# Kernel optimization log

Measured on AMD Instinct MI355X. Metric: run time of the kernel, lower is better.

## Reference

```python
import jax, jax.numpy as jnp
import numpy as np

TAU = 1.0          # temperature
PAD = -1.0         # padded_value_indicator
MAX_ITER = 50      # sinkhorn iterations
NEG_BIG = -100000000.0


def setup_inputs() -> dict:
    key = jax.random.key(0)
    k1, k2 = jax.random.split(key)
    B, N = 128, 256
    y_pred = jax.random.normal(k1, (B, N), dtype=jnp.float32)
    y_true = jax.random.randint(k2, (B, N), 0, 5, dtype=jnp.int32)
    return {"y_pred": y_pred, "y_true": y_true}


def deterministic_neural_sort(s, tau, mask):
    # s: [B, n, 1], mask: [B, n] bool
    B, n = s.shape[0], s.shape[1]
    mor = mask[:, :, None] | mask[:, None, :]
    mand = mask[:, :, None] & mask[:, None, :]
    s = jnp.where(mask[:, :, None], NEG_BIG, s)
    A_s = jnp.abs(s - jnp.swapaxes(s, 1, 2))            # [B, n, n]
    A_s = jnp.where(mor, 0.0, A_s)
    # B_mat[b,i,j] = sum_k A_s[b,i,k] (matmul with ones outer product)
    B_mat = A_s.sum(axis=2, keepdims=True)              # [B, n, 1], broadcasts over j
    m = mask.sum(axis=1)                                # [B] number of padded items
    j = jnp.arange(n)
    valid = j[None, :] < (n - m)[:, None]
    scaling = jnp.where(
        valid,
        (n - m)[:, None].astype(jnp.float32) + 1.0 - 2.0 * (j[None, :] + 1).astype(jnp.float32),
        0.0,
    )                                                   # [B, n]
    s0 = jnp.where(mask[:, :, None], 0.0, s)
    C = s0 * scaling[:, None, :]                        # [B,n,1]*[B,1,n] outer product
    P_max = jnp.swapaxes(C - B_mat, 1, 2)
    P_max = jnp.where(mor, -jnp.inf, P_max)
    P_max = jnp.where(mand, 1.0, P_max)
    return jax.nn.softmax(P_max / tau, axis=-1)         # [B, n, n]


def sinkhorn_scaling(mat, mask):
    # mat: [B, n, n], mask: [B, n]
    mor = mask[:, None, :] | mask[:, :, None]
    mand = mask[:, None, :] & mask[:, :, None]
    mat = jnp.where(mor, 0.0, mat)
    mat = jnp.where(mand, 1.0, mat)

    def step(m, _):
        m = m / jnp.clip(m.sum(axis=1, keepdims=True), 1e-10, None)
        m = m / jnp.clip(m.sum(axis=2, keepdims=True), 1e-10, None)
        return m, None

    mat, _ = jax.lax.scan(step, mat, None, length=MAX_ITER)
    return jnp.where(mor, 0.0, mat)


def dcg_at_k(y_pred, y_true, k, gain_fn):
    # returns [B, 1]
    mask = y_true == PAD
    yp = jnp.where(mask, -jnp.inf, y_pred)
    yt = jnp.where(mask, 0.0, y_true)
    order = jnp.argsort(-yp, axis=-1)
    sorted_true = jnp.take_along_axis(yt, order, axis=-1)
    n = y_true.shape[1]
    disc = 1.0 / jnp.log2(jnp.arange(n, dtype=jnp.float32) + 2.0)
    cum = jnp.cumsum(gain_fn(sorted_true) * disc, axis=1)[:, :k]
    return cum[:, k - 1 : k]


def reference(y_pred, y_true):
    B, n = y_pred.shape
    yt = y_true.astype(jnp.float32)
    yt = yt.max() - yt + yt.min()            # relevancy flip as in source
    k = n                                    # self.k is None
    mask = yt == PAD

    P_hat = deterministic_neural_sort(y_pred[:, :, None], TAU, mask)  # [B,n,n]
    P_hat = sinkhorn_scaling(P_hat, mask)[None]                        # [1,B,n,n]
    mor = mask[None, :, :, None] | mask[None, :, None, :]
    P_hat = jnp.where(mor, 0.0, P_hat)

    yt_masked = jnp.where(mask, 0.0, yt)
    gains = jnp.power(2.0, yt_masked) - 1.0                            # powered_relevancies
    ground_truth = jnp.einsum('sbij,bj->sbi', P_hat, gains)            # [1,B,n]
    disc = 1.0 / jnp.log2(jnp.arange(n, dtype=jnp.float32) + 2.0)
    discounted_gains = ground_truth * disc

    idcg = dcg_at_k(yt, yt, k, lambda x: jnp.power(2.0, x) - 1.0).T    # [1,B]
    ndcg = discounted_gains[:, :, :k].sum(axis=-1) / (idcg + 1e-10)    # [1,B]
    idcg_mask = idcg == 0.0
    ndcg = jnp.where(idcg_mask, 0.0, ndcg)
    cnt = (~idcg_mask).sum()
    mean_ndcg = ndcg.sum() / jnp.maximum(cnt.astype(jnp.float32) * ndcg.shape[0], 1.0)
    return jnp.where(cnt > 0, -mean_ndcg, 0.0)
```

## Files before the change

kernel.cpp:

```cpp
#include <hip/hip_runtime.h>


#define NN 256

template<int C>
__device__ __forceinline__ float dppmov(float v) {
    return __int_as_float(__builtin_amdgcn_update_dpp(0, __float_as_int(v), C, 0xF, 0xF, true));
}
__device__ __forceinline__ float swz16(float v) {
    return __int_as_float(__builtin_amdgcn_ds_swizzle(__float_as_int(v), 0x401F));
}
__device__ __forceinline__ float sum32(float v) {
    v += dppmov<0xB1>(v);
    v += dppmov<0x4E>(v);
    v += dppmov<0x141>(v);
    v += dppmov<0x140>(v);
    v += swz16(v);
    return v;
}
__device__ __forceinline__ float max32(float v) {
    v = fmaxf(v, dppmov<0xB1>(v));
    v = fmaxf(v, dppmov<0x4E>(v));
    v = fmaxf(v, dppmov<0x141>(v));
    v = fmaxf(v, dppmov<0x140>(v));
    v = fmaxf(v, swz16(v));
    return v;
}
__device__ __forceinline__ float sum4(float v) {
    v += dppmov<0xB1>(v);
    v += dppmov<0x4E>(v);
    return v;
}

__global__ void minmax_kernel(const int* __restrict__ yt, int n, int* __restrict__ wsi) {
    int t = blockIdx.x * blockDim.x + threadIdx.x;
    int mn = 0x7f7f7f7f, mx = (int)0x80808080;
    for (int i = t; i < n; i += gridDim.x * blockDim.x) {
        int v = yt[i];
        mn = min(mn, v);
        mx = max(mx, v);
    }
    for (int m = 32; m; m >>= 1) {
        mn = min(mn, __shfl_xor(mn, m));
        mx = max(mx, __shfl_xor(mx, m));
    }
    __shared__ int smn[4], smx[4];
    int w = threadIdx.x >> 6;
    if ((threadIdx.x & 63) == 0) { smn[w] = mn; smx[w] = mx; }
    __syncthreads();
    if (threadIdx.x == 0) {
        for (int i = 1; i < 4; ++i) { mn = min(mn, smn[i]); mx = max(mx, smx[i]); }
        atomicMin(&wsi[0], mn);
        atomicMax(&wsi[1], mx);
    }
}

__global__ __launch_bounds__(1024, 4) void ndcg_main(const float* __restrict__ yp,
                                                     const int* __restrict__ ytr,
                                                     const int* __restrict__ wsi,
                                                     float* __restrict__ wsf) {
    const int b = blockIdx.x;
    const int t = threadIdx.x;
    const int l = t & 63;
    const int ti = t >> 5;
    const int tj = t & 31;

    __shared__ float4 part4[32 * 64];
    __shared__ float4 colinv4[64];
    __shared__ __align__(16) float s[NN], Bm[NN], g[NN], disc[NN];
    __shared__ float numAcc, idcgAcc;
    __shared__ int hist[64];

    const int ymin = wsi[0];
    const int ymax = wsi[1];
    float* partf = (float*)part4;

    int ytv = 0;
    if (t < 64) hist[t] = 0;
    if (t < NN) {
        s[t] = yp[b * NN + t];
        int yv = ytr[b * NN + t];
        ytv = ymax - yv + ymin;
        g[t] = exp2f((float)ytv) - 1.0f;
        disc[t] = 1.0f / log2f((float)t + 2.0f);
    }
    if (t == 0) { numAcc = 0.0f; idcgAcc = 0.0f; }
    __syncthreads();

    {
        int j = t & 255, q = t >> 8;
        float sv = s[j];
        float acc = 0.0f;
        int k0 = q * 64;
#pragma unroll 8
        for (int k = 0; k < 64; ++k) acc += fabsf(sv - s[k0 + k]);
        partf[q * 256 + j] = acc;
    }
    __syncthreads();
    if (t < NN) {
        Bm[t] = partf[t] + partf[256 + t] + partf[512 + t] + partf[768 + t];
        int bin = min(max(ytv - ymin, 0), 63);
        atomicAdd(&hist[bin], 1);
    }
    __syncthreads();

    float m[8][8];
    {
        float sj[8], bmj[8];
        ((float4*)sj)[0] = ((float4*)s)[tj * 2];
        ((float4*)sj)[1] = ((float4*)s)[tj * 2 + 1];
        ((float4*)bmj)[0] = ((float4*)Bm)[tj * 2];
        ((float4*)bmj)[1] = ((float4*)Bm)[tj * 2 + 1];
#pragma unroll
        for (int a = 0; a < 8; ++a) {
            float sc = (float)(255 - 2 * (ti * 8 + a));
#pragma unroll
            for (int bb = 0; bb < 8; ++bb) m[a][bb] = sj[bb] * sc - bmj[bb];
            float mx = fmaxf(fmaxf(fmaxf(m[a][0], m[a][1]), fmaxf(m[a][2], m[a][3])),
                             fmaxf(fmaxf(m[a][4], m[a][5]), fmaxf(m[a][6], m[a][7])));
            mx = max32(mx);
            float z = 0.0f;
#pragma unroll
            for (int bb = 0; bb < 8; ++bb) { m[a][bb] = expf(m[a][bb] - mx); z += m[a][bb]; }
            z = sum32(z);
            float rz = __builtin_amdgcn_rcpf(z);
#pragma unroll
            for (int bb = 0; bb < 8; ++bb) m[a][bb] *= rz;
        }
    }

    const int wslot = ti * 64 + ((tj + ti) & 31);
    const int csj = t >> 2, csq = t & 3;
    const int csc = csj >> 3, csd = csj & 7;
    const int civ_idx = ((csd & 4) ? 128 : 0) + 4 * csc + (csd & 3);

    for (int it = 0; it < 50; ++it) {
        float p[8];
#pragma unroll
        for (int bb = 0; bb < 8; ++bb)
            p[bb] = ((m[0][bb] + m[1][bb]) + (m[2][bb] + m[3][bb])) +
                    ((m[4][bb] + m[5][bb]) + (m[6][bb] + m[7][bb]));
        part4[wslot]      = make_float4(p[0], p[1], p[2], p[3]);
        part4[wslot + 32] = make_float4(p[4], p[5], p[6], p[7]);
        __syncthreads();

        {
            float cs = 0.0f;
#pragma unroll
            for (int k = 0; k < 8; ++k) {
                int ss = 4 * k + csq;
                int slotr = ss * 64 + ((csc + ss) & 31) + ((csd & 4) ? 32 : 0);
                cs += partf[slotr * 4 + (csd & 3)];
            }
            cs = sum4(cs);
            float civ = __builtin_amdgcn_rcpf(fmaxf(cs, 1e-10f));
            if (csq == 0) ((float*)colinv4)[civ_idx] = civ;
        }
        __syncthreads();

        float cv[8];
        ((float4*)cv)[0] = colinv4[tj];
        ((float4*)cv)[1] = colinv4[32 + tj];
#pragma unroll
        for (int a = 0; a < 8; ++a) {
            float racc = 0.0f;
#pragma unroll
            for (int bb = 0; bb < 8; ++bb) { m[a][bb] *= cv[bb]; racc += m[a][bb]; }
            racc = sum32(racc);
            float ri = __builtin_amdgcn_rcpf(fmaxf(racc, 1e-10f));
#pragma unroll
            for (int bb = 0; bb < 8; ++bb) m[a][bb] *= ri;
        }
    }

    {
        float gv[8];
        ((float4*)gv)[0] = ((float4*)g)[tj * 2];
        ((float4*)gv)[1] = ((float4*)g)[tj * 2 + 1];
        float partial = 0.0f;
#pragma unroll
        for (int a = 0; a < 8; ++a) {
            float acc = 0.0f;
#pragma unroll
            for (int bb = 0; bb < 8; ++bb) acc += m[a][bb] * gv[bb];
            acc = sum32(acc);
            partial += disc[ti * 8 + a] * acc;
        }
        if ((l & 31) == 0) atomicAdd(&numAcc, partial);
    }

    __syncthreads();
    if (t < NN) {
        int p = t;
        float gain_p = 0.0f;
        int off = 0;
        for (int vb = 63; vb >= 0; --vb) {
            int c = hist[vb];
            if (p >= off && p < off + c) gain_p = exp2f((float)(vb + ymin)) - 1.0f;
            off += c;
        }
        float contrib = disc[p] * gain_p;
        contrib = sum32(contrib);
        contrib += __shfl_xor(contrib, 32);
        if (t == 0 || t == 64 || t == 128 || t == 192)
            atomicAdd(&idcgAcc, contrib * 0.0f + __shfl_xor(contrib, 0) * 0.0f + contrib);
    }
    __syncthreads();

    if (t == 0) {
        float idcg = idcgAcc;
        float nd = (idcg != 0.0f) ? numAcc / (idcg + 1e-10f) : 0.0f;
        atomicAdd(&wsf[0], nd);
        if (idcg != 0.0f) atomicAdd(&wsf[1], 1.0f);
    }
}

__global__ void finalize_kernel(const float* __restrict__ wsf, float* __restrict__ out) {
    if (threadIdx.x == 0) {
        float sum = wsf[0];
        float cnt = wsf[1];
        out[0] = (cnt > 0.0f) ? -(sum / fmaxf(cnt, 1.0f)) : 0.0f;
    }
}

extern "C" void kernel_launch(void* const* d_in, const int* in_sizes, int n_in,
                              void* d_out, int out_size, void* d_ws, size_t ws_size,
                              hipStream_t stream) {
    const float* y_pred = (const float*)d_in[0];
    const int* y_true = (const int*)d_in[1];
    const int total = in_sizes[0];
    const int B = total / NN;

    int* wsi = (int*)d_ws;
    float* wsf = (float*)((char*)d_ws + 8);

    hipMemsetAsync(wsi, 0x7f, 4, stream);
    hipMemsetAsync(wsi + 1, 0x80, 4, stream);
    hipMemsetAsync(wsf, 0, 8, stream);
    minmax_kernel<<<128, 256, 0, stream>>>(y_true, total, wsi);
    ndcg_main<<<B, 1024, 0, stream>>>(y_pred, y_true, wsi, wsf);
    finalize_kernel<<<1, 64, 0, stream>>>(wsf, (float*)d_out);
}
```

Before: 179.9 us.

## Rewrite Sinkhorn as implicit row/column scaling vectors with fused minmax

```diff
diff --git a/kernel.cpp b/kernel.cpp
--- a/kernel.cpp
+++ b/kernel.cpp
@@ -2,224 +2,273 @@
 
 
 #define NN 256
+#define ITERS 50
 
 template<int C>
-__device__ __forceinline__ float dppmov(float v) {
-    return __int_as_float(__builtin_amdgcn_update_dpp(0, __float_as_int(v), C, 0xF, 0xF, true));
-}
-__device__ __forceinline__ float swz16(float v) {
-    return __int_as_float(__builtin_amdgcn_ds_swizzle(__float_as_int(v), 0x401F));
-}
-__device__ __forceinline__ float sum32(float v) {
-    v += dppmov<0xB1>(v);
-    v += dppmov<0x4E>(v);
-    v += dppmov<0x141>(v);
-    v += dppmov<0x140>(v);
-    v += swz16(v);
+__device__ __forceinline__ float dppadd(float v) {
+    return v + __int_as_float(__builtin_amdgcn_update_dpp(0, __float_as_int(v), C, 0xF, 0xF, true));
+}
+template<int C>
+__device__ __forceinline__ float dppmax(float v) {
+    return fmaxf(v, __int_as_float(__builtin_amdgcn_update_dpp(0, __float_as_int(v), C, 0xF, 0xF, true)));
+}
+__device__ __forceinline__ float sum8(float v) {
+    v = dppadd<0xB1>(v);
+    v = dppadd<0x4E>(v);
+    v = dppadd<0x141>(v);
     return v;
 }
-__device__ __forceinline__ float max32(float v) {
-    v = fmaxf(v, dppmov<0xB1>(v));
-    v = fmaxf(v, dppmov<0x4E>(v));
-    v = fmaxf(v, dppmov<0x141>(v));
-    v = fmaxf(v, dppmov<0x140>(v));
-    v = fmaxf(v, swz16(v));
+__device__ __forceinline__ float sum16(float v) {
+    v = dppadd<0xB1>(v);
+    v = dppadd<0x4E>(v);
+    v = dppadd<0x141>(v);
+    v = dppadd<0x140>(v);
     return v;
 }
-__device__ __forceinline__ float sum4(float v) {
-    v += dppmov<0xB1>(v);
-    v += dppmov<0x4E>(v);
+__device__ __forceinline__ float max16(float v) {
+    v = dppmax<0xB1>(v);
+    v = dppmax<0x4E>(v);
+    v = dppmax<0x141>(v);
+    v = dppmax<0x140>(v);
     return v;
 }
 
-__global__ void minmax_kernel(const int* __restrict__ yt, int n, int* __restrict__ wsi) {
-    int t = blockIdx.x * blockDim.x + threadIdx.x;
-    int mn = 0x7f7f7f7f, mx = (int)0x80808080;
-    for (int i = t; i < n; i += gridDim.x * blockDim.x) {
-        int v = yt[i];
-        mn = min(mn, v);
-        mx = max(mx, v);
-    }
-    for (int m = 32; m; m >>= 1) {
-        mn = min(mn, __shfl_xor(mn, m));
-        mx = max(mx, __shfl_xor(mx, m));
-    }
-    __shared__ int smn[4], smx[4];
-    int w = threadIdx.x >> 6;
-    if ((threadIdx.x & 63) == 0) { smn[w] = mn; smx[w] = mx; }
-    __syncthreads();
-    if (threadIdx.x == 0) {
-        for (int i = 1; i < 4; ++i) { mn = min(mn, smn[i]); mx = max(mx, smx[i]); }
-        atomicMin(&wsi[0], mn);
-        atomicMax(&wsi[1], mx);
-    }
-}
-
-__global__ __launch_bounds__(1024, 4) void ndcg_main(const float* __restrict__ yp,
-                                                     const int* __restrict__ ytr,
-                                                     const int* __restrict__ wsi,
-                                                     float* __restrict__ wsf) {
+__global__ __launch_bounds__(512, 2) void ndcg_main(const float* __restrict__ yp,
+                                                    const int* __restrict__ ytr,
+                                                    int nbatch,
+                                                    float* __restrict__ ndOut,
+                                                    float* __restrict__ cntOut) {
     const int b = blockIdx.x;
     const int t = threadIdx.x;
-    const int l = t & 63;
-    const int ti = t >> 5;
-    const int tj = t & 31;
-
-    __shared__ float4 part4[32 * 64];
-    __shared__ float4 colinv4[64];
-    __shared__ __align__(16) float s[NN], Bm[NN], g[NN], disc[NN];
+    const int ti = t >> 4;
+    const int tj = t & 15;
+    const int cg = t >> 3;
+    const int sb = t & 7;
+
+    __shared__ float4 part4[32 * 65];
+    __shared__ float4 cvec4[64];
+    __shared__ float4 bm4[64];
+    __shared__ __align__(16) float sarr[NN], garr[NN], darr[NN];
     __shared__ float numAcc, idcgAcc;
-    __shared__ int hist[64];
-
-    const int ymin = wsi[0];
-    const int ymax = wsi[1];
-    float* partf = (float*)part4;
-
-    int ytv = 0;
+    __shared__ int hist[64], wmn[8], wmx[8], gmn, gmx;
+
+    {
+        int mn = 0x7fffffff, mx = (int)0x80000000;
+        const int4* y4 = (const int4*)ytr;
+        const int n4 = nbatch * (NN / 4);
+        for (int i = t; i < n4; i += 512) {
+            int4 v = y4[i];
+            mn = min(mn, min(min(v.x, v.y), min(v.z, v.w)));
+            mx = max(mx, max(max(v.x, v.y), max(v.z, v.w)));
+        }
+        for (int mo = 1; mo < 64; mo <<= 1) {
+            mn = min(mn, __shfl_xor(mn, mo));
+            mx = max(mx, __shfl_xor(mx, mo));
+        }
+        if ((t & 63) == 0) { wmn[t >> 6] = mn; wmx[t >> 6] = mx; }
+    }
     if (t < 64) hist[t] = 0;
+    if (t == 0) { numAcc = 0.0f; idcgAcc = 0.0f; }
+    __syncthreads();
+    if (t == 0) {
+        int a = wmn[0], c = wmx[0];
+        for (int i = 1; i < 8; ++i) { a = min(a, wmn[i]); c = max(c, wmx[i]); }
+        gmn = a; gmx = c;
+    }
+    __syncthreads();
+    const int ymin = gmn, ymax = gmx;
+
     if (t < NN) {
-        s[t] = yp[b * NN + t];
-        int yv = ytr[b * NN + t];
-        ytv = ymax - yv + ymin;
-        g[t] = exp2f((float)ytv) - 1.0f;
-        disc[t] = 1.0f / log2f((float)t + 2.0f);
-    }
-    if (t == 0) { numAcc = 0.0f; idcgAcc = 0.0f; }
-    __syncthreads();
-
-    {
-        int j = t & 255, q = t >> 8;
-        float sv = s[j];
-        float acc = 0.0f;
-        int k0 = q * 64;
-#pragma unroll 8
-        for (int k = 0; k < 64; ++k) acc += fabsf(sv - s[k0 + k]);
-        partf[q * 256 + j] = acc;
-    }
-    __syncthreads();
-    if (t < NN) {
-        Bm[t] = partf[t] + partf[256 + t] + partf[512 + t] + partf[768 + t];
-        int bin = min(max(ytv - ymin, 0), 63);
-        atomicAdd(&hist[bin], 1);
-    }
-    __syncthreads();
-
-    float m[8][8];
-    {
-        float sj[8], bmj[8];
-        ((float4*)sj)[0] = ((float4*)s)[tj * 2];
-        ((float4*)sj)[1] = ((float4*)s)[tj * 2 + 1];
-        ((float4*)bmj)[0] = ((float4*)Bm)[tj * 2];
-        ((float4*)bmj)[1] = ((float4*)Bm)[tj * 2 + 1];
+        sarr[t] = yp[b * NN + t];
+        int ytv = ymax - ytr[b * NN + t] + ymin;
+        garr[t] = exp2f((float)ytv) - 1.0f;
+        darr[t] = 1.0f / log2f((float)t + 2.0f);
+        ((float*)cvec4)[t] = 1.0f;
+        atomicAdd(&hist[min(max(ytv - ymin, 0), 63)], 1);
+    }
+    __syncthreads();
+
+    float sj[16], si[8];
+    {
+        const float4* s4 = (const float4*)sarr;
+        *(float4*)&sj[0]  = s4[tj * 4 + 0];
+        *(float4*)&sj[4]  = s4[tj * 4 + 1];
+        *(float4*)&sj[8]  = s4[tj * 4 + 2];
+        *(float4*)&sj[12] = s4[tj * 4 + 3];
+        *(float4*)&si[0]  = s4[ti * 2 + 0];
+        *(float4*)&si[4]  = s4[ti * 2 + 1];
+    }
+
+    const int pbase = ti * 65 + tj * 4;
+
+    {
+        float p[16];
+#pragma unroll
+        for (int bb = 0; bb < 16; ++bb) {
+            float acc = 0.0f;
+#pragma unroll
+            for (int a = 0; a < 8; ++a) acc += fabsf(sj[bb] - si[a]);
+            p[bb] = acc;
+        }
+#pragma unroll
+        for (int k = 0; k < 4; ++k)
+            part4[pbase + k] = make_float4(p[4 * k], p[4 * k + 1], p[4 * k + 2], p[4 * k + 3]);
+        __syncthreads();
+        float4 S0 = part4[sb * 65 + cg];
+        float4 S1 = part4[(sb + 8) * 65 + cg];
+        float4 S2 = part4[(sb + 16) * 65 + cg];
+        float4 S3 = part4[(sb + 24) * 65 + cg];
+        float4 S = make_float4(S0.x + S1.x + S2.x + S3.x, S0.y + S1.y + S2.y + S3.y,
+                               S0.z + S1.z + S2.z + S3.z, S0.w + S1.w + S2.w + S3.w);
+        S.x = sum8(S.x); S.y = sum8(S.y); S.z = sum8(S.z); S.w = sum8(S.w);
+        if (sb == 0) bm4[cg] = S;
+        __syncthreads();
+    }
+
+    float m[8][16];
+    {
+        float bmj[16];
+        *(float4*)&bmj[0]  = bm4[tj * 4 + 0];
+        *(float4*)&bmj[4]  = bm4[tj * 4 + 1];
+        *(float4*)&bmj[8]  = bm4[tj * 4 + 2];
+        *(float4*)&bmj[12] = bm4[tj * 4 + 3];
 #pragma unroll
         for (int a = 0; a < 8; ++a) {
             float sc = (float)(255 - 2 * (ti * 8 + a));
-#pragma unroll
-            for (int bb = 0; bb < 8; ++bb) m[a][bb] = sj[bb] * sc - bmj[bb];
-            float mx = fmaxf(fmaxf(fmaxf(m[a][0], m[a][1]), fmaxf(m[a][2], m[a][3])),
-                             fmaxf(fmaxf(m[a][4], m[a][5]), fmaxf(m[a][6], m[a][7])));
-            mx = max32(mx);
+            float mx = -3.0e38f;
+#pragma unroll
+            for (int bb = 0; bb < 16; ++bb) {
+                m[a][bb] = sj[bb] * sc - bmj[bb];
+                mx = fmaxf(mx, m[a][bb]);
+            }
+            mx = max16(mx);
             float z = 0.0f;
 #pragma unroll
-            for (int bb = 0; bb < 8; ++bb) { m[a][bb] = expf(m[a][bb] - mx); z += m[a][bb]; }
-            z = sum32(z);
+            for (int bb = 0; bb < 16; ++bb) { m[a][bb] = expf(m[a][bb] - mx); z += m[a][bb]; }
+            z = sum16(z);
             float rz = __builtin_amdgcn_rcpf(z);
 #pragma unroll
-            for (int bb = 0; bb < 8; ++bb) m[a][bb] *= rz;
-        }
-    }
-
-    const int wslot = ti * 64 + ((tj + ti) & 31);
-    const int csj = t >> 2, csq = t & 3;
-    const int csc = csj >> 3, csd = csj & 7;
-    const int civ_idx = ((csd & 4) ? 128 : 0) + 4 * csc + (csd & 3);
-
-    for (int it = 0; it < 50; ++it) {
-        float p[8];
-#pragma unroll
-        for (int bb = 0; bb < 8; ++bb)
-            p[bb] = ((m[0][bb] + m[1][bb]) + (m[2][bb] + m[3][bb])) +
-                    ((m[4][bb] + m[5][bb]) + (m[6][bb] + m[7][bb]));
-        part4[wslot]      = make_float4(p[0], p[1], p[2], p[3]);
-        part4[wslot + 32] = make_float4(p[4], p[5], p[6], p[7]);
-        __syncthreads();
-
-        {
-            float cs = 0.0f;
-#pragma unroll
-            for (int k = 0; k < 8; ++k) {
-                int ss = 4 * k + csq;
-                int slotr = ss * 64 + ((csc + ss) & 31) + ((csd & 4) ? 32 : 0);
-                cs += partf[slotr * 4 + (csd & 3)];
-            }
-            cs = sum4(cs);
-            float civ = __builtin_amdgcn_rcpf(fmaxf(cs, 1e-10f));
-            if (csq == 0) ((float*)colinv4)[civ_idx] = civ;
-        }
-        __syncthreads();
-
-        float cv[8];
-        ((float4*)cv)[0] = colinv4[tj];
-        ((float4*)cv)[1] = colinv4[32 + tj];
-#pragma unroll
-        for (int a = 0; a < 8; ++a) {
-            float racc = 0.0f;
-#pragma unroll
-            for (int bb = 0; bb < 8; ++bb) { m[a][bb] *= cv[bb]; racc += m[a][bb]; }
-            racc = sum32(racc);
-            float ri = __builtin_amdgcn_rcpf(fmaxf(racc, 1e-10f));
-#pragma unroll
-            for (int bb = 0; bb < 8; ++bb) m[a][bb] *= ri;
-        }
-    }
-
-    {
-        float gv[8];
-        ((float4*)gv)[0] = ((float4*)g)[tj * 2];
-        ((float4*)gv)[1] = ((float4*)g)[tj * 2 + 1];
-        float partial = 0.0f;
-#pragma unroll
-        for (int a = 0; a < 8; ++a) {
-            float acc = 0.0f;
-#pragma unroll
-            for (int bb = 0; bb < 8; ++bb) acc += m[a][bb] * gv[bb];
-            acc = sum32(acc);
-            partial += disc[ti * 8 + a] * acc;
-        }
-        if ((l & 31) == 0) atomicAdd(&numAcc, partial);
-    }
-
-    __syncthreads();
+            for (int bb = 0; bb < 16; ++bb) m[a][bb] *= rz;
+        }
+    }
+
     if (t < NN) {
-        int p = t;
         float gain_p = 0.0f;
         int off = 0;
         for (int vb = 63; vb >= 0; --vb) {
             int c = hist[vb];
-            if (p >= off && p < off + c) gain_p = exp2f((float)(vb + ymin)) - 1.0f;
+            if (t >= off && t < off + c) gain_p = exp2f((float)(vb + ymin)) - 1.0f;
             off += c;
         }
-        float contrib = disc[p] * gain_p;
-        contrib = sum32(contrib);
+        float contrib = darr[t] * gain_p;
+        contrib = sum16(contrib);
+        contrib += __shfl_xor(contrib, 16);
         contrib += __shfl_xor(contrib, 32);
-        if (t == 0 || t == 64 || t == 128 || t == 192)
-            atomicAdd(&idcgAcc, contrib * 0.0f + __shfl_xor(contrib, 0) * 0.0f + contrib);
+        if ((t & 63) == 0) atomicAdd(&idcgAcc, contrib);
+    }
+
+    float r[8];
+#pragma unroll
+    for (int a = 0; a < 8; ++a) r[a] = 1.0f;
+
+    for (int it = 0; it < ITERS; ++it) {
+        float p[16];
+#pragma unroll
+        for (int bb = 0; bb < 16; ++bb) {
+            float acc = m[0][bb] * r[0];
+#pragma unroll
+            for (int a = 1; a < 8; ++a) acc = fmaf(m[a][bb], r[a], acc);
+            p[bb] = acc;
+        }
+#pragma unroll
+        for (int k = 0; k < 4; ++k)
+            part4[pbase + k] = make_float4(p[4 * k], p[4 * k + 1], p[4 * k + 2], p[4 * k + 3]);
+        __syncthreads();
+
+        {
+            float4 S0 = part4[sb * 65 + cg];
+            float4 S1 = part4[(sb + 8) * 65 + cg];
+            float4 S2 = part4[(sb + 16) * 65 + cg];
+            float4 S3 = part4[(sb + 24) * 65 + cg];
+            float4 S = make_float4(S0.x + S1.x + S2.x + S3.x, S0.y + S1.y + S2.y + S3.y,
+                                   S0.z + S1.z + S2.z + S3.z, S0.w + S1.w + S2.w + S3.w);
+            S.x = sum8(S.x); S.y = sum8(S.y); S.z = sum8(S.z); S.w = sum8(S.w);
+            if (sb == 0) {
+                float4 cO = cvec4[cg];
+                float4 cN;
+                cN.x = fminf((cO.x * S.x < 1e-10f) ? cO.x * 1e10f : __builtin_amdgcn_rcpf(S.x), 1e37f);
+                cN.y = fminf((cO.y * S.y < 1e-10f) ? cO.y * 1e10f : __builtin_amdgcn_rcpf(S.y), 1e37f);
+                cN.z = fminf((cO.z * S.z < 1e-10f) ? cO.z * 1e10f : __builtin_amdgcn_rcpf(S.z), 1e37f);
+                cN.w = fminf((cO.w * S.w < 1e-10f) ? cO.w * 1e10f : __builtin_amdgcn_rcpf(S.w), 1e37f);
+                cvec4[cg] = cN;
+            }
+        }
+        __syncthreads();
+
+        {
+            float cv[16];
+            *(float4*)&cv[0]  = cvec4[tj * 4 + 0];
+            *(float4*)&cv[4]  = cvec4[tj * 4 + 1];
+            *(float4*)&cv[8]  = cvec4[tj * 4 + 2];
+            *(float4*)&cv[12] = cvec4[tj * 4 + 3];
+#pragma unroll
+            for (int a = 0; a < 8; ++a) {
+                float acc = m[a][0] * cv[0];
+#pragma unroll
+                for (int bb = 1; bb < 16; ++bb) acc = fmaf(m[a][bb], cv[bb], acc);
+                float T = sum16(acc);
+                float rs = r[a] * T;
+                float rn = (rs < 1e-10f) ? r[a] * 1e10f : __builtin_amdgcn_rcpf(T);
+                r[a] = fminf(rn, 1e37f);
+            }
+        }
+    }
+
+    {
+        float wv[16];
+#pragma unroll
+        for (int k = 0; k < 4; ++k) {
+            float4 cV = cvec4[tj * 4 + k];
+            float4 gV = ((const float4*)garr)[tj * 4 + k];
+            wv[4 * k + 0] = cV.x * gV.x;
+            wv[4 * k + 1] = cV.y * gV.y;
+            wv[4 * k + 2] = cV.z * gV.z;
+            wv[4 * k + 3] = cV.w * gV.w;
+        }
+        float partial = 0.0f;
+#pragma unroll
+        for (int a = 0; a < 8; ++a) {
+            float acc = m[a][0] * wv[0];
+#pragma unroll
+            for (int bb = 1; bb < 16; ++bb) acc = fmaf(m[a][bb], wv[bb], acc);
+            float T = sum16(acc);
+            partial = fmaf(darr[ti * 8 + a] * r[a], T, partial);
+        }
+        if (tj == 0) atomicAdd(&numAcc, partial);
     }
     __syncthreads();
 
     if (t == 0) {
         float idcg = idcgAcc;
-        float nd = (idcg != 0.0f) ? numAcc / (idcg + 1e-10f) : 0.0f;
-        atomicAdd(&wsf[0], nd);
-        if (idcg != 0.0f) atomicAdd(&wsf[1], 1.0f);
-    }
-}
-
-__global__ void finalize_kernel(const float* __restrict__ wsf, float* __restrict__ out) {
-    if (threadIdx.x == 0) {
-        float sum = wsf[0];
-        float cnt = wsf[1];
-        out[0] = (cnt > 0.0f) ? -(sum / fmaxf(cnt, 1.0f)) : 0.0f;
+        bool ok = (idcg != 0.0f);
+        ndOut[b] = ok ? numAcc / (idcg + 1e-10f) : 0.0f;
+        cntOut[b] = ok ? 1.0f : 0.0f;
+    }
+}
+
+__global__ void finalize_kernel(const float* __restrict__ ndArr,
+                                const float* __restrict__ cntArr,
+                                int nbatch, float* __restrict__ out) {
+    int t = threadIdx.x;
+    float s = 0.0f, c = 0.0f;
+    for (int i = t; i < nbatch; i += 128) { s += ndArr[i]; c += cntArr[i]; }
+    for (int mo = 1; mo < 64; mo <<= 1) { s += __shfl_xor(s, mo); c += __shfl_xor(c, mo); }
+    __shared__ float s2[2], c2[2];
+    if ((t & 63) == 0) { s2[t >> 6] = s; c2[t >> 6] = c; }
+    __syncthreads();
+    if (t == 0) {
+        float S = s2[0] + s2[1], C = c2[0] + c2[1];
+        out[0] = (C > 0.0f) ? -(S / fmaxf(C, 1.0f)) : 0.0f;
     }
 }
 
@@ -231,13 +280,9 @@
     const int total = in_sizes[0];
     const int B = total / NN;
 
-    int* wsi = (int*)d_ws;
-    float* wsf = (float*)((char*)d_ws + 8);
-
-    hipMemsetAsync(wsi, 0x7f, 4, stream);
-    hipMemsetAsync(wsi + 1, 0x80, 4, stream);
-    hipMemsetAsync(wsf, 0, 8, stream);
-    minmax_kernel<<<128, 256, 0, stream>>>(y_true, total, wsi);
-    ndcg_main<<<B, 1024, 0, stream>>>(y_pred, y_true, wsi, wsf);
-    finalize_kernel<<<1, 64, 0, stream>>>(wsf, (float*)d_out);
-}
+    float* ndArr = (float*)d_ws;
+    float* cntArr = ndArr + B;
+
+    ndcg_main<<<B, 512, 0, stream>>>(y_pred, y_true, B, ndArr, cntArr);
+    finalize_kernel<<<1, 128, 0, stream>>>(ndArr, cntArr, B, (float*)d_out);
+}
```

After: 268.9 us. +49.4%, slower.
